# Optimization experiments

Hardware: AMD Instinct MI355X
Metric: run time of the kernel (lower is better)

Reference implementation:

```python
import jax, jax.numpy as jnp
import numpy as np

LOW_A, LOW_B = 32 // 4, 32 // 4  # spatial_shape=(32,32) default -> keep 8x8 low freqs


def _dct_basis(K, N, dtype):
    # Unnormalized DCT-II basis (torch_dct norm=None): C[k,n] = 2*cos(pi*(2n+1)k/(2N))
    n = jnp.arange(N, dtype=jnp.float32)
    k = jnp.arange(K, dtype=jnp.float32)
    return (2.0 * jnp.cos(jnp.pi * (2.0 * n[None, :] + 1.0) * k[:, None] / (2.0 * N))).astype(dtype)


def setup_inputs() -> dict:
    key = jax.random.key(0)
    delta = jax.random.normal(key, (256, 3, 256, 256), dtype=jnp.float32)
    return {"delta": delta}


def reference(delta):
    B, C, H, W = delta.shape
    Ch = _dct_basis(LOW_A, H, delta.dtype)  # [a, H]
    Cw = _dct_basis(LOW_B, W, delta.dtype)  # [b, W]
    # Equivalent to dct_2d(delta)[:, :, :a, :b]: truncated DCT along H then W.
    low = jnp.einsum('ih,nchw,jw->ncij', Ch, delta, Cw)  # [B, C, a, b]
    return jnp.abs(low).mean()
```

## Files before the change

kernel.cpp:

```cpp
#include <hip/hip_runtime.h>


#define INV_COUNT (1.0f / 49152.0f)

__global__ __launch_bounds__(256) void lowfreq_main(
    const float* __restrict__ delta, float* __restrict__ out)
{
    __shared__ __align__(16) float c_row[256][8];
    __shared__ __align__(16) float c_col[8][260];
    __shared__ __align__(16) float u_lds[8][260];
    __shared__ float pacc[4][64];

    const int t = threadIdx.x;
    const int wave = t >> 6;
    const int lane = t & 63;

    {
        const float a = 3.14159265358979323846f * (2.0f * (float)t + 1.0f)
                        * (1.0f / 512.0f);
        const float ca = cosf(a);
        float ckm1 = 1.0f, ck = ca;
        c_row[t][0] = 2.0f;       c_col[0][t] = 2.0f;
        c_row[t][1] = 2.0f * ca;  c_col[1][t] = 2.0f * ca;
        #pragma unroll
        for (int k = 2; k < 8; ++k) {
            const float cn = 2.0f * ca * ck - ckm1;
            ckm1 = ck; ck = cn;
            c_row[t][k] = 2.0f * cn;
            c_col[k][t] = 2.0f * cn;
        }
    }
    __syncthreads();

    const int row0 = wave << 6;
    const float* gp = delta + (size_t)blockIdx.x * 65536
                            + (size_t)row0 * 256 + lane;

    float u[4][8];
    #pragma unroll
    for (int c = 0; c < 4; ++c)
        #pragma unroll
        for (int i = 0; i < 8; ++i) u[c][i] = 0.0f;

    #pragma unroll 4
    for (int r = 0; r < 64; ++r) {
        const int h = row0 + r;
        const float x0 = gp[r * 256 + 0];
        const float x1 = gp[r * 256 + 64];
        const float x2 = gp[r * 256 + 128];
        const float x3 = gp[r * 256 + 192];
        const float4 cA = *reinterpret_cast<const float4*>(&c_row[h][0]);
        const float4 cB = *reinterpret_cast<const float4*>(&c_row[h][4]);
        const float cc[8] = {cA.x, cA.y, cA.z, cA.w, cB.x, cB.y, cB.z, cB.w};
        #pragma unroll
        for (int i = 0; i < 8; ++i) {
            u[0][i] = fmaf(cc[i], x0, u[0][i]);
            u[1][i] = fmaf(cc[i], x1, u[1][i]);
            u[2][i] = fmaf(cc[i], x2, u[2][i]);
            u[3][i] = fmaf(cc[i], x3, u[3][i]);
        }
    }

    #pragma unroll
    for (int s = 0; s < 4; ++s) {
        if (wave == s) {
            #pragma unroll
            for (int i = 0; i < 8; ++i)
                #pragma unroll
                for (int c = 0; c < 4; ++c) {
                    const int w = (c << 6) + lane;
                    if (s == 0) u_lds[i][w] = u[c][i];
                    else        u_lds[i][w] += u[c][i];
                }
        }
        __syncthreads();
    }

    {
        const int i = lane >> 3;
        const int j = lane & 7;
        const int w0 = wave << 6;
        float acc = 0.0f;
        #pragma unroll
        for (int k = 0; k < 16; ++k) {
            const float4 uv = *reinterpret_cast<const float4*>(&u_lds[i][w0 + (k << 2)]);
            const float4 cv = *reinterpret_cast<const float4*>(&c_col[j][w0 + (k << 2)]);
            acc = fmaf(uv.x, cv.x, acc);
            acc = fmaf(uv.y, cv.y, acc);
            acc = fmaf(uv.z, cv.z, acc);
            acc = fmaf(uv.w, cv.w, acc);
        }
        pacc[wave][lane] = acc;
    }
    __syncthreads();

    if (wave == 0) {
        const float s4 = pacc[0][lane] + pacc[1][lane]
                       + pacc[2][lane] + pacc[3][lane];
        float a = fabsf(s4);
        #pragma unroll
        for (int m = 1; m < 64; m <<= 1) a += __shfl_xor(a, m, 64);
        if (lane == 0) atomicAdd(out, a * INV_COUNT);
    }
}

extern "C" void kernel_launch(void* const* d_in, const int* in_sizes, int n_in,
                              void* d_out, int out_size, void* d_ws, size_t ws_size,
                              hipStream_t stream)
{
    const float* delta = (const float*)d_in[0];
    float* out = (float*)d_out;
    hipMemsetAsync(out, 0, 4, stream);
    lowfreq_main<<<768, 256, 0, stream>>>(delta, out);
}
```

Before: 48.76 us.

## Split each image across two blocks, prefetch rows early, and reduce in second kernel

```diff
diff --git a/kernel.cpp b/kernel.cpp
--- a/kernel.cpp
+++ b/kernel.cpp
@@ -4,7 +4,8 @@
 #define INV_COUNT (1.0f / 49152.0f)
 
 __global__ __launch_bounds__(256) void lowfreq_main(
-    const float* __restrict__ delta, float* __restrict__ out)
+    const float* __restrict__ delta, float* __restrict__ ws,
+    float* __restrict__ out)
 {
     __shared__ __align__(16) float c_row[256][8];
     __shared__ __align__(16) float c_col[8][260];
@@ -14,6 +15,20 @@
     const int t = threadIdx.x;
     const int wave = t >> 6;
     const int lane = t & 63;
+    const int bid = blockIdx.x;
+    const int img = bid >> 1;
+    const int half = bid & 1;
+
+    const int row0 = (half << 7) + (wave << 5);
+    const float* gp = delta + (size_t)img * 65536 + (size_t)row0 * 256 + lane;
+
+    float x[4][4];
+    #pragma unroll
+    for (int rr = 0; rr < 4; ++rr) {
+        const float* p = gp + (size_t)rr * 256;
+        x[rr][0] = p[0];  x[rr][1] = p[64];
+        x[rr][2] = p[128]; x[rr][3] = p[192];
+    }
 
     {
         const float a = 3.14159265358979323846f * (2.0f * (float)t + 1.0f)
@@ -32,32 +47,43 @@
     }
     __syncthreads();
 
-    const int row0 = wave << 6;
-    const float* gp = delta + (size_t)blockIdx.x * 65536
-                            + (size_t)row0 * 256 + lane;
-
     float u[4][8];
     #pragma unroll
     for (int c = 0; c < 4; ++c)
         #pragma unroll
         for (int i = 0; i < 8; ++i) u[c][i] = 0.0f;
 
-    #pragma unroll 4
-    for (int r = 0; r < 64; ++r) {
-        const int h = row0 + r;
-        const float x0 = gp[r * 256 + 0];
-        const float x1 = gp[r * 256 + 64];
-        const float x2 = gp[r * 256 + 128];
-        const float x3 = gp[r * 256 + 192];
-        const float4 cA = *reinterpret_cast<const float4*>(&c_row[h][0]);
-        const float4 cB = *reinterpret_cast<const float4*>(&c_row[h][4]);
-        const float cc[8] = {cA.x, cA.y, cA.z, cA.w, cB.x, cB.y, cB.z, cB.w};
+    #pragma unroll
+    for (int rb = 0; rb < 8; ++rb) {
+        float xn[4][4];
+        if (rb < 7) {
+            #pragma unroll
+            for (int rr = 0; rr < 4; ++rr) {
+                const float* p = gp + (size_t)((rb + 1) * 4 + rr) * 256;
+                xn[rr][0] = p[0];  xn[rr][1] = p[64];
+                xn[rr][2] = p[128]; xn[rr][3] = p[192];
+            }
+        }
         #pragma unroll
-        for (int i = 0; i < 8; ++i) {
-            u[0][i] = fmaf(cc[i], x0, u[0][i]);
-            u[1][i] = fmaf(cc[i], x1, u[1][i]);
-            u[2][i] = fmaf(cc[i], x2, u[2][i]);
-            u[3][i] = fmaf(cc[i], x3, u[3][i]);
+        for (int rr = 0; rr < 4; ++rr) {
+            const int h = row0 + (rb << 2) + rr;
+            const float4 cA = *reinterpret_cast<const float4*>(&c_row[h][0]);
+            const float4 cB = *reinterpret_cast<const float4*>(&c_row[h][4]);
+            const float cc[8] = {cA.x, cA.y, cA.z, cA.w, cB.x, cB.y, cB.z, cB.w};
+            #pragma unroll
+            for (int i = 0; i < 8; ++i) {
+                u[0][i] = fmaf(cc[i], x[rr][0], u[0][i]);
+                u[1][i] = fmaf(cc[i], x[rr][1], u[1][i]);
+                u[2][i] = fmaf(cc[i], x[rr][2], u[2][i]);
+                u[3][i] = fmaf(cc[i], x[rr][3], u[3][i]);
+            }
+        }
+        if (rb < 7) {
+            #pragma unroll
+            for (int rr = 0; rr < 4; ++rr)
+                #pragma unroll
+                for (int c = 0; c < 4; ++c)
+                    x[rr][c] = xn[rr][c];
         }
     }
 
@@ -97,11 +123,31 @@
     if (wave == 0) {
         const float s4 = pacc[0][lane] + pacc[1][lane]
                        + pacc[2][lane] + pacc[3][lane];
-        float a = fabsf(s4);
-        #pragma unroll
-        for (int m = 1; m < 64; m <<= 1) a += __shfl_xor(a, m, 64);
-        if (lane == 0) atomicAdd(out, a * INV_COUNT);
+        ws[(size_t)bid * 64 + lane] = s4;
+        if (bid == 0 && lane == 0) out[0] = 0.0f;
     }
+}
+
+__global__ __launch_bounds__(256) void lowfreq_reduce(
+    const float* __restrict__ ws, float* __restrict__ out)
+{
+    __shared__ float acc[4];
+    const int t = threadIdx.x;
+    const int wave = t >> 6;
+    const int lane = t & 63;
+    const int g = blockIdx.x * 256 + t;
+    const int img = g >> 6;
+    const int slot = g & 63;
+
+    const float s = ws[(size_t)(2 * img) * 64 + slot]
+                  + ws[(size_t)(2 * img + 1) * 64 + slot];
+    float a = fabsf(s);
+    #pragma unroll
+    for (int m = 1; m < 64; m <<= 1) a += __shfl_xor(a, m, 64);
+    if (lane == 0) acc[wave] = a;
+    __syncthreads();
+    if (t == 0)
+        atomicAdd(out, (acc[0] + acc[1] + acc[2] + acc[3]) * INV_COUNT);
 }
 
 extern "C" void kernel_launch(void* const* d_in, const int* in_sizes, int n_in,
@@ -110,6 +156,7 @@
 {
     const float* delta = (const float*)d_in[0];
     float* out = (float*)d_out;
-    hipMemsetAsync(out, 0, 4, stream);
-    lowfreq_main<<<768, 256, 0, stream>>>(delta, out);
+    float* ws = (float*)d_ws;
+    lowfreq_main<<<1536, 256, 0, stream>>>(delta, ws, out);
+    lowfreq_reduce<<<192, 256, 0, stream>>>(ws, out);
 }
```

Result: faster. 41.53 us (-14.8%).
